# Optimization experiments

Hardware: AMD Instinct MI355X
Metric: run time of the kernel (lower is better)

## Reference

```python
import jax, jax.numpy as jnp
import numpy as np

B, T_HIST, D_IN = 4096, 60, 2
H, L, T_OUT = 128, 2, 360


def _lstm_cell(x, h, c, Wih, Whh, b):
    # PyTorch gate order: i, f, g, o
    z = x @ Wih.T + h @ Whh.T + b  # (B, 4H)
    i, f, g, o = jnp.split(z, 4, axis=-1)
    c_new = jax.nn.sigmoid(f) * c + jax.nn.sigmoid(i) * jnp.tanh(g)
    h_new = jax.nn.sigmoid(o) * jnp.tanh(c_new)
    return h_new, c_new


def _multilayer_step(x_t, hs, cs, Wih, Whh, b):
    # hs, cs: (L, B, H); Wih: (L, 4H, H); Whh: (L, 4H, H); b: (L, 4H)
    new_h, new_c = [], []
    inp = x_t
    for l in range(L):
        h, c = _lstm_cell(inp, hs[l], cs[l], Wih[l], Whh[l], b[l])
        new_h.append(h)
        new_c.append(c)
        inp = h
    return inp, jnp.stack(new_h), jnp.stack(new_c)


def setup_inputs() -> dict:
    key = jax.random.key(0)
    ks = jax.random.split(key, 14)
    s = 0.1
    inp = {
        "history": jax.random.normal(ks[0], (B, T_HIST, D_IN), jnp.float32),
        "emb_W": jax.random.normal(ks[1], (H, D_IN), jnp.float32) * s,
        "emb_b": jax.random.normal(ks[2], (H,), jnp.float32) * s,
        "enc_Wih": jax.random.normal(ks[3], (L, 4 * H, H), jnp.float32) * s,
        "enc_Whh": jax.random.normal(ks[4], (L, 4 * H, H), jnp.float32) * s,
        "enc_bih": jax.random.normal(ks[5], (L, 4 * H), jnp.float32) * s,
        "enc_bhh": jax.random.normal(ks[6], (L, 4 * H), jnp.float32) * s,
        "dec_Wih": jax.random.normal(ks[7], (L, 4 * H, H), jnp.float32) * s,
        "dec_Whh": jax.random.normal(ks[8], (L, 4 * H, H), jnp.float32) * s,
        "dec_bih": jax.random.normal(ks[9], (L, 4 * H), jnp.float32) * s,
        "dec_bhh": jax.random.normal(ks[10], (L, 4 * H), jnp.float32) * s,
        "out_W": jax.random.normal(ks[11], (D_IN, H), jnp.float32) * s,
        "out_b": jax.random.normal(ks[12], (D_IN,), jnp.float32) * s,
    }
    return inp


def reference(history, emb_W, emb_b, enc_Wih, enc_Whh, enc_bih, enc_bhh,
              dec_Wih, dec_Whh, dec_bih, dec_bhh, out_W, out_b):
    batch = history.shape[0]
    enc_b = enc_bih + enc_bhh  # (L, 4H)
    dec_b = dec_bih + dec_bhh

    # input embedding: (B, T, 2) -> (B, T, H)
    hist_embed = history @ emb_W.T + emb_b

    # --- encoder LSTM (eval mode, no dropout) ---
    h0 = jnp.zeros((L, batch, H), hist_embed.dtype)
    c0 = jnp.zeros((L, batch, H), hist_embed.dtype)

    def enc_step(carry, x_t):
        hs, cs = carry
        _, hs, cs = _multilayer_step(x_t, hs, cs, enc_Wih, enc_Whh, enc_b)
        return (hs, cs), None

    (h_n, c_n), _ = jax.lax.scan(enc_step, (h0, c0),
                                 jnp.transpose(hist_embed, (1, 0, 2)))  # scan over time

    dec_in0 = jnp.zeros((batch, H), hist_embed.dtype)

    def dec_step(carry, _):
        dec_in, hs, cs = carry
        top, hs, cs = _multilayer_step(dec_in, hs, cs, dec_Wih, dec_Whh, dec_b)
        pred = top @ out_W.T + out_b              # (B, 2)
        nxt = pred @ emb_W.T + emb_b              # re-embed prediction
        return (nxt, hs, cs), pred

    _, preds = jax.lax.scan(dec_step, (dec_in0, h_n, c_n), None, length=T_OUT)
    return jnp.transpose(preds, (1, 0, 2))  # (B, T_OUT, 2)
```

## Files before the change

### kernel.cpp

```cpp
#include <hip/hip_runtime.h>
#include <stdint.h>

#define NT 512

typedef __attribute__((ext_vector_type(8))) __bf16 bf16x8;
typedef __attribute__((ext_vector_type(8))) unsigned short ushort8;
typedef __attribute__((ext_vector_type(4))) float f32x4;

static __device__ __forceinline__ unsigned short f2bf(float f) {
    union { float f; uint32_t u; } v; v.f = f;
    uint32_t r = v.u + 0x7fffu + ((v.u >> 16) & 1u);
    return (unsigned short)(r >> 16);
}
static __device__ __forceinline__ float sigm(float x) {
    return __builtin_amdgcn_rcpf(1.0f + __expf(-x));
}
static __device__ __forceinline__ float tanh_(float x) {
    return 2.0f * __builtin_amdgcn_rcpf(1.0f + __expf(-2.0f * x)) - 1.0f;
}
static __device__ __forceinline__ bf16x8 ld8(const unsigned short* p) {
    return __builtin_bit_cast(bf16x8, *(const ushort8*)p);
}
static __device__ __forceinline__ float swz(float v, int imm) {
    int r;
    if (imm == 0x0010) r = __builtin_amdgcn_ds_swizzle(__builtin_bit_cast(int, v), 0x0010);
    else               r = __builtin_amdgcn_ds_swizzle(__builtin_bit_cast(int, v), 0x0410);
    return __builtin_bit_cast(float, r);
}

__global__ void prep_kernel(
    const float* __restrict__ emb_W, const float* __restrict__ emb_b,
    const float* __restrict__ enc_Wih, const float* __restrict__ enc_Whh,
    const float* __restrict__ dec_Wih, const float* __restrict__ dec_Whh,
    const float* __restrict__ enc_bih, const float* __restrict__ enc_bhh,
    const float* __restrict__ dec_bih, const float* __restrict__ dec_bhh,
    unsigned short* __restrict__ W0p, unsigned short* __restrict__ W1p,
    float* __restrict__ benc, float* __restrict__ bdec,
    float* __restrict__ Me, float* __restrict__ Md,
    float* __restrict__ ve, float* __restrict__ vd)
{
    int idx = blockIdx.x * blockDim.x + threadIdx.x;
    if (idx < 2 * 512 * 256) {
        int net = idx >> 17;
        int rem = idx & 131071;
        int n = rem >> 8, k = rem & 255;
        const float* Wih = net ? dec_Wih : enc_Wih;
        const float* Whh = net ? dec_Whh : enc_Whh;
        float v = (k < 128) ? Wih[(size_t)(512 + n) * 128 + k]
                            : Whh[(size_t)(512 + n) * 128 + k - 128];
        W1p[(size_t)net * 131072 + rem] = f2bf(v);
    }
    if (idx < 2 * 512 * 128) {
        int net = idx >> 16;
        int rem = idx & 65535;
        int j = rem & 7, quad = (rem >> 3) & 3, ln = (rem >> 5) & 15;
        int w = (rem >> 9) & 7, g = (rem >> 12) & 3, c = (rem >> 14) & 3;
        int n = g * 128 + w * 16 + ln;
        int k = c * 32 + quad * 8 + j;
        const float* Whh = net ? dec_Whh : enc_Whh;
        W0p[(size_t)net * 65536 + rem] = f2bf(Whh[(size_t)n * 128 + k]);
    }
    if (idx < 2048) {
        int net = idx >> 10;
        int rem = idx & 1023;
        float v = net ? (dec_bih[rem] + dec_bhh[rem]) : (enc_bih[rem] + enc_bhh[rem]);
        (net ? bdec : benc)[rem] = v;
    }
    if (idx < 1024) {
        int net = idx >> 9, n = idx & 511;
        const float* Wih = net ? dec_Wih : enc_Wih;
        float m0 = 0.f, m1 = 0.f, vv = 0.f;
        for (int k = 0; k < 128; ++k) {
            float wv = Wih[(size_t)n * 128 + k];
            m0 += wv * emb_W[k * 2 + 0];
            m1 += wv * emb_W[k * 2 + 1];
            vv += wv * emb_b[k];
        }
        float* M = net ? Md : Me;
        float* V = net ? vd : ve;
        M[n * 2 + 0] = m0; M[n * 2 + 1] = m1; V[n] = vv;
    }
}

__global__ __launch_bounds__(NT, 2) void lstm_kernel(
    const float* __restrict__ hist,
    const unsigned short* __restrict__ W0p, const unsigned short* __restrict__ W1p,
    const float* __restrict__ benc, const float* __restrict__ bdec,
    const float* __restrict__ Me, const float* __restrict__ Md,
    const float* __restrict__ ve, const float* __restrict__ vd,
    const float* __restrict__ out_W, const float* __restrict__ out_b,
    float* __restrict__ out)
{
    __shared__ __align__(16) unsigned short A1s[2 * 4096];
    __shared__ __align__(16) unsigned short W0Ls[65536];
    __shared__ __align__(16) float histL[16 * 120];

    const int tid = threadIdx.x;
    const int lane = tid & 63;
    const int w = tid >> 6;
    const int ln = lane & 15;
    const int quad = lane >> 4;
    const int row0 = blockIdx.x * 16;
    const int cc0 = w * 16 + ln;
    const int cg = (cc0 >> 3) & 3;

    const unsigned short* a1r = A1s + ln * 32 + ((quad ^ ((ln >> 2) & 3)) * 8);
    unsigned short* a1w = A1s + (cc0 >> 5) * 512 + quad * 128 + ((cg ^ quad) * 8) + (ln & 7);
    const unsigned short* w0b[4];
#pragma unroll
    for (int c = 0; c < 4; ++c)
        w0b[c] = W0Ls + c * 16384 + w * 512 + ln * 32 + quad * 8;

    for (int e = tid; e < 1024; e += NT) ((uint4*)A1s)[e] = make_uint4(0u, 0u, 0u, 0u);
    for (int e = tid; e < 480; e += NT)
        ((float4*)histL)[e] = ((const float4*)(hist + (size_t)row0 * 120))[e];

    const int nidx = (ln < 2) ? ln : 0;
    const float outbL = out_b[nidx];
    bf16x8 ow[4];
#pragma unroll
    for (int c = 0; c < 4; ++c) {
        unsigned short tmp[8];
#pragma unroll
        for (int j = 0; j < 8; ++j)
            tmp[j] = f2bf(out_W[nidx * 128 + c * 32 + quad * 8 + j]);
        ow[c] = __builtin_bit_cast(bf16x8, *(ushort8*)tmp);
    }

    bf16x8 wl[4][8];
    float b0c[4], bvc[4], b1c[4], M0c[4], M1c[4];
    float c0r[4] = {0.f, 0.f, 0.f, 0.f};
    float c1r[4] = {0.f, 0.f, 0.f, 0.f};

    auto load_consts = [&](const float* bb, const float* M, const float* V,
                           const unsigned short* W1) {
#pragma unroll
        for (int g = 0; g < 4; ++g) {
            const int n = g * 128 + cc0;
#pragma unroll
            for (int q = 0; q < 8; ++q)
                wl[g][q] = ld8(W1 + (size_t)n * 256 + quad * 8 + q * 32);
            b0c[g] = bb[n];
            b1c[g] = bb[512 + n];
            M0c[g] = M[n * 2 + 0];
            M1c[g] = M[n * 2 + 1];
            bvc[g] = bb[n] + V[n];
        }
    };
    auto copy_w0 = [&](const unsigned short* src) {
        for (int e = tid; e < 8192; e += NT)
            ((uint4*)W0Ls)[e] = ((const uint4*)src)[e];
    };

    copy_w0(W0p);
    load_consts(benc, Me, ve, W1p);
    __syncthreads();

    auto enc_step = [&](int t, int buf) {
        bf16x8 a0[4];
#pragma unroll
        for (int c = 0; c < 4; ++c)
            a0[c] = ld8(a1r + (buf ^ 1) * 4096 + c * 512);
        f32x4 acc[4];
#pragma unroll
        for (int g = 0; g < 4; ++g)
#pragma unroll
            for (int i = 0; i < 4; ++i) {
                float2 pv = *(const float2*)&histL[(quad * 4 + i) * 120 + 2 * t];
                acc[g][i] = bvc[g] + M0c[g] * pv.x + M1c[g] * pv.y;
            }
#pragma unroll
        for (int c = 0; c < 4; ++c)
#pragma unroll
            for (int g = 0; g < 4; ++g)
                acc[g] = __builtin_amdgcn_mfma_f32_16x16x32_bf16(a0[c], ld8(w0b[c] + g * 4096), acc[g], 0, 0, 0);
#pragma unroll
        for (int i = 0; i < 4; ++i) {
            float iv = sigm(acc[0][i]);
            float fv = sigm(acc[1][i]);
            float gv = tanh_(acc[2][i]);
            float ov = sigm(acc[3][i]);
            c0r[i] = fv * c0r[i] + iv * gv;
            a1w[buf * 4096 + i * 32] = f2bf(ov * tanh_(c0r[i]));
        }
        __syncthreads();
        f32x4 acc1[4];
#pragma unroll
        for (int g = 0; g < 4; ++g)
#pragma unroll
            for (int i = 0; i < 4; ++i) acc1[g][i] = b1c[g];
#pragma unroll
        for (int q = 0; q < 8; ++q) {
            bf16x8 af = ld8(a1r + buf * 4096 + q * 512);
#pragma unroll
            for (int g = 0; g < 4; ++g)
                acc1[g] = __builtin_amdgcn_mfma_f32_16x16x32_bf16(af, wl[g][q], acc1[g], 0, 0, 0);
        }
#pragma unroll
        for (int i = 0; i < 4; ++i) {
            float iv = sigm(acc1[0][i]);
            float fv = sigm(acc1[1][i]);
            float gv = tanh_(acc1[2][i]);
            float ov = sigm(acc1[3][i]);
            c1r[i] = fv * c1r[i] + iv * gv;
            a1w[(buf ^ 1) * 4096 + 2048 + i * 32] = f2bf(ov * tanh_(c1r[i]));
        }
        __syncthreads();
    };

    for (int t = 0; t < 60; t += 2) { enc_step(t, 0); enc_step(t + 1, 1); }

    copy_w0(W0p + 65536);
    load_consts(bdec, Md, vd, W1p + 131072);
    __syncthreads();

    auto dec_step = [&](int d, int buf) {
        f32x4 acc[4];
        if (d > 0) {
            f32x4 pacc = {0.f, 0.f, 0.f, 0.f};
#pragma unroll
            for (int c = 0; c < 4; ++c) {
                bf16x8 ah = ld8(a1r + buf * 4096 + (4 + c) * 512);
                pacc = __builtin_amdgcn_mfma_f32_16x16x32_bf16(ah, ow[c], pacc, 0, 0, 0);
            }
            float pd[4];
#pragma unroll
            for (int i = 0; i < 4; ++i) pd[i] = pacc[i] + outbL;
            if (w == 0 && ln < 2) {
#pragma unroll
                for (int i = 0; i < 4; ++i)
                    out[(size_t)(row0 + quad * 4 + i) * 720 + (size_t)(d - 1) * 2 + ln] = pd[i];
            }
#pragma unroll
            for (int g = 0; g < 4; ++g)
#pragma unroll
                for (int i = 0; i < 4; ++i) acc[g][i] = bvc[g];
#pragma unroll
            for (int i = 0; i < 4; ++i) {
                float p0 = swz(pd[i], 0x0010);
                float p1 = swz(pd[i], 0x0410);
#pragma unroll
                for (int g = 0; g < 4; ++g)
                    acc[g][i] += M0c[g] * p0 + M1c[g] * p1;
            }
        } else {
#pragma unroll
            for (int g = 0; g < 4; ++g)
#pragma unroll
                for (int i = 0; i < 4; ++i) acc[g][i] = b0c[g];
        }
        bf16x8 a0[4];
#pragma unroll
        for (int c = 0; c < 4; ++c)
            a0[c] = ld8(a1r + (buf ^ 1) * 4096 + c * 512);
#pragma unroll
        for (int c = 0; c < 4; ++c)
#pragma unroll
            for (int g = 0; g < 4; ++g)
                acc[g] = __builtin_amdgcn_mfma_f32_16x16x32_bf16(a0[c], ld8(w0b[c] + g * 4096), acc[g], 0, 0, 0);
#pragma unroll
        for (int i = 0; i < 4; ++i) {
            float iv = sigm(acc[0][i]);
            float fv = sigm(acc[1][i]);
            float gv = tanh_(acc[2][i]);
            float ov = sigm(acc[3][i]);
            c0r[i] = fv * c0r[i] + iv * gv;
            a1w[buf * 4096 + i * 32] = f2bf(ov * tanh_(c0r[i]));
        }
        __syncthreads();
        f32x4 acc1[4];
#pragma unroll
        for (int g = 0; g < 4; ++g)
#pragma unroll
            for (int i = 0; i < 4; ++i) acc1[g][i] = b1c[g];
#pragma unroll
        for (int q = 0; q < 8; ++q) {
            bf16x8 af = ld8(a1r + buf * 4096 + q * 512);
#pragma unroll
            for (int g = 0; g < 4; ++g)
                acc1[g] = __builtin_amdgcn_mfma_f32_16x16x32_bf16(af, wl[g][q], acc1[g], 0, 0, 0);
        }
#pragma unroll
        for (int i = 0; i < 4; ++i) {
            float iv = sigm(acc1[0][i]);
            float fv = sigm(acc1[1][i]);
            float gv = tanh_(acc1[2][i]);
            float ov = sigm(acc1[3][i]);
            c1r[i] = fv * c1r[i] + iv * gv;
            a1w[(buf ^ 1) * 4096 + 2048 + i * 32] = f2bf(ov * tanh_(c1r[i]));
        }
        __syncthreads();
    };

    for (int d = 0; d < 360; d += 2) { dec_step(d, 0); dec_step(d + 1, 1); }

    {
        f32x4 pacc = {0.f, 0.f, 0.f, 0.f};
#pragma unroll
        for (int c = 0; c < 4; ++c) {
            bf16x8 ah = ld8(a1r + 0 * 4096 + (4 + c) * 512);
            pacc = __builtin_amdgcn_mfma_f32_16x16x32_bf16(ah, ow[c], pacc, 0, 0, 0);
        }
        if (w == 0 && ln < 2) {
#pragma unroll
            for (int i = 0; i < 4; ++i)
                out[(size_t)(row0 + quad * 4 + i) * 720 + 359 * 2 + ln] = pacc[i] + outbL;
        }
    }
}

extern "C" void kernel_launch(void* const* d_in, const int* in_sizes, int n_in,
                              void* d_out, int out_size, void* d_ws, size_t ws_size,
                              hipStream_t stream) {
    const float* hist    = (const float*)d_in[0];
    const float* emb_W   = (const float*)d_in[1];
    const float* emb_b   = (const float*)d_in[2];
    const float* enc_Wih = (const float*)d_in[3];
    const float* enc_Whh = (const float*)d_in[4];
    const float* enc_bih = (const float*)d_in[5];
    const float* enc_bhh = (const float*)d_in[6];
    const float* dec_Wih = (const float*)d_in[7];
    const float* dec_Whh = (const float*)d_in[8];
    const float* dec_bih = (const float*)d_in[9];
    const float* dec_bhh = (const float*)d_in[10];
    const float* out_W   = (const float*)d_in[11];
    const float* out_b   = (const float*)d_in[12];

    char* ws = (char*)d_ws;
    unsigned short* W0p = (unsigned short*)(ws + 0);
    unsigned short* W1p = (unsigned short*)(ws + 262144);
    float* benc = (float*)(ws + 786432);
    float* bdec = (float*)(ws + 790528);
    float* Me   = (float*)(ws + 794624);
    float* Md   = (float*)(ws + 798720);
    float* ve   = (float*)(ws + 802816);
    float* vd   = (float*)(ws + 804864);

    prep_kernel<<<1024, 256, 0, stream>>>(emb_W, emb_b,
                                          enc_Wih, enc_Whh, dec_Wih, dec_Whh,
                                          enc_bih, enc_bhh, dec_bih, dec_bhh,
                                          W0p, W1p, benc, bdec, Me, Md, ve, vd);
    lstm_kernel<<<256, NT, 0, stream>>>(hist, W0p, W1p,
                                        benc, bdec, Me, Md, ve, vd,
                                        out_W, out_b, (float*)d_out);
}
```

Measured before the change: 1.214 ms.

## Skew LSTM layers across timesteps and swizzle layer-0 weight LDS layout

Restructures the recurrence so each step computes layer 1 at time t and layer 0 at time t+1 from the same loaded hidden-state fragments. In the encoder this removes one barrier per step. The decoder keeps two barriers per step, but the layer-0 weight MFMA now overlaps the layer-1 work and only the small projection and embedding fixup stays on the serial path. It also XOR-swizzles the layer-0 weight layout in LDS to reduce bank conflicts, and adds prologue and epilogue code for the skewed schedule, which raises complexity and the chance of indexing errors.

```diff
diff --git a/kernel.cpp b/kernel.cpp
--- a/kernel.cpp
+++ b/kernel.cpp
@@ -109,9 +109,9 @@
     const unsigned short* w0b[4];
 #pragma unroll
     for (int c = 0; c < 4; ++c)
-        w0b[c] = W0Ls + c * 16384 + w * 512 + ln * 32 + quad * 8;
-
-    for (int e = tid; e < 1024; e += NT) ((uint4*)A1s)[e] = make_uint4(0u, 0u, 0u, 0u);
+        w0b[c] = W0Ls + c * 16384 + w * 512 + ln * 32 + ((quad ^ ((ln >> 1) & 3)) * 8);
+
+    for (int e = tid; e < 256; e += NT) ((uint4*)A1s)[256 + e] = make_uint4(0u, 0u, 0u, 0u);
     for (int e = tid; e < 480; e += NT)
         ((float4*)histL)[e] = ((const float4*)(hist + (size_t)row0 * 120))[e];
 
@@ -148,54 +148,64 @@
         }
     };
     auto copy_w0 = [&](const unsigned short* src) {
-        for (int e = tid; e < 8192; e += NT)
-            ((uint4*)W0Ls)[e] = ((const uint4*)src)[e];
+        for (int e = tid; e < 8192; e += NT) {
+            int d = (e & ~3) | ((e & 3) ^ ((e >> 3) & 3));
+            ((uint4*)W0Ls)[d] = ((const uint4*)src)[e];
+        }
     };
 
     copy_w0(W0p);
     load_consts(benc, Me, ve, W1p);
     __syncthreads();
 
+    {
+        f32x4 z[4];
+#pragma unroll
+        for (int i = 0; i < 4; ++i) {
+            float x0 = hist[(size_t)(row0 + quad * 4 + i) * 120 + 0];
+            float x1 = hist[(size_t)(row0 + quad * 4 + i) * 120 + 1];
+#pragma unroll
+            for (int g = 0; g < 4; ++g) z[g][i] = bvc[g] + M0c[g] * x0 + M1c[g] * x1;
+        }
+#pragma unroll
+        for (int i = 0; i < 4; ++i) {
+            float iv = sigm(z[0][i]);
+            float gv = tanh_(z[2][i]);
+            float ov = sigm(z[3][i]);
+            c0r[i] = iv * gv;
+            a1w[i * 32] = f2bf(ov * tanh_(c0r[i]));
+        }
+    }
+    __syncthreads();
+
     auto enc_step = [&](int t, int buf) {
-        bf16x8 a0[4];
+        bf16x8 af[8];
+#pragma unroll
+        for (int q = 0; q < 8; ++q)
+            af[q] = ld8(a1r + buf * 4096 + q * 512);
+        f32x4 acc1[4];
+#pragma unroll
+        for (int g = 0; g < 4; ++g)
+#pragma unroll
+            for (int i = 0; i < 4; ++i) acc1[g][i] = b1c[g];
+#pragma unroll
+        for (int q = 0; q < 8; ++q)
+#pragma unroll
+            for (int g = 0; g < 4; ++g)
+                acc1[g] = __builtin_amdgcn_mfma_f32_16x16x32_bf16(af[q], wl[g][q], acc1[g], 0, 0, 0);
+        f32x4 acc0[4];
+#pragma unroll
+        for (int g = 0; g < 4; ++g)
+#pragma unroll
+            for (int i = 0; i < 4; ++i) {
+                float2 pv = *(const float2*)&histL[(quad * 4 + i) * 120 + 2 * (t + 1)];
+                acc0[g][i] = bvc[g] + M0c[g] * pv.x + M1c[g] * pv.y;
+            }
 #pragma unroll
         for (int c = 0; c < 4; ++c)
-            a0[c] = ld8(a1r + (buf ^ 1) * 4096 + c * 512);
-        f32x4 acc[4];
-#pragma unroll
-        for (int g = 0; g < 4; ++g)
-#pragma unroll
-            for (int i = 0; i < 4; ++i) {
-                float2 pv = *(const float2*)&histL[(quad * 4 + i) * 120 + 2 * t];
-                acc[g][i] = bvc[g] + M0c[g] * pv.x + M1c[g] * pv.y;
-            }
-#pragma unroll
-        for (int c = 0; c < 4; ++c)
-#pragma unroll
-            for (int g = 0; g < 4; ++g)
-                acc[g] = __builtin_amdgcn_mfma_f32_16x16x32_bf16(a0[c], ld8(w0b[c] + g * 4096), acc[g], 0, 0, 0);
-#pragma unroll
-        for (int i = 0; i < 4; ++i) {
-            float iv = sigm(acc[0][i]);
-            float fv = sigm(acc[1][i]);
-            float gv = tanh_(acc[2][i]);
-            float ov = sigm(acc[3][i]);
-            c0r[i] = fv * c0r[i] + iv * gv;
-            a1w[buf * 4096 + i * 32] = f2bf(ov * tanh_(c0r[i]));
-        }
-        __syncthreads();
-        f32x4 acc1[4];
-#pragma unroll
-        for (int g = 0; g < 4; ++g)
-#pragma unroll
-            for (int i = 0; i < 4; ++i) acc1[g][i] = b1c[g];
-#pragma unroll
-        for (int q = 0; q < 8; ++q) {
-            bf16x8 af = ld8(a1r + buf * 4096 + q * 512);
-#pragma unroll
-            for (int g = 0; g < 4; ++g)
-                acc1[g] = __builtin_amdgcn_mfma_f32_16x16x32_bf16(af, wl[g][q], acc1[g], 0, 0, 0);
-        }
+#pragma unroll
+            for (int g = 0; g < 4; ++g)
+                acc0[g] = __builtin_amdgcn_mfma_f32_16x16x32_bf16(af[c], ld8(w0b[c] + g * 4096), acc0[g], 0, 0, 0);
 #pragma unroll
         for (int i = 0; i < 4; ++i) {
             float iv = sigm(acc1[0][i]);
@@ -205,81 +215,91 @@
             c1r[i] = fv * c1r[i] + iv * gv;
             a1w[(buf ^ 1) * 4096 + 2048 + i * 32] = f2bf(ov * tanh_(c1r[i]));
         }
+#pragma unroll
+        for (int i = 0; i < 4; ++i) {
+            float iv = sigm(acc0[0][i]);
+            float fv = sigm(acc0[1][i]);
+            float gv = tanh_(acc0[2][i]);
+            float ov = sigm(acc0[3][i]);
+            c0r[i] = fv * c0r[i] + iv * gv;
+            a1w[(buf ^ 1) * 4096 + i * 32] = f2bf(ov * tanh_(c0r[i]));
+        }
         __syncthreads();
     };
 
-    for (int t = 0; t < 60; t += 2) { enc_step(t, 0); enc_step(t + 1, 1); }
-
-    copy_w0(W0p + 65536);
-    load_consts(bdec, Md, vd, W1p + 131072);
-    __syncthreads();
+    for (int t = 0; t < 58; t += 2) { enc_step(t, 0); enc_step(t + 1, 1); }
+    enc_step(58, 0);
+
+    {
+        bf16x8 af[8];
+#pragma unroll
+        for (int q = 0; q < 8; ++q)
+            af[q] = ld8(a1r + 4096 + q * 512);
+        f32x4 acc1[4];
+#pragma unroll
+        for (int g = 0; g < 4; ++g)
+#pragma unroll
+            for (int i = 0; i < 4; ++i) acc1[g][i] = b1c[g];
+#pragma unroll
+        for (int q = 0; q < 8; ++q)
+#pragma unroll
+            for (int g = 0; g < 4; ++g)
+                acc1[g] = __builtin_amdgcn_mfma_f32_16x16x32_bf16(af[q], wl[g][q], acc1[g], 0, 0, 0);
+#pragma unroll
+        for (int i = 0; i < 4; ++i) {
+            float iv = sigm(acc1[0][i]);
+            float fv = sigm(acc1[1][i]);
+            float gv = tanh_(acc1[2][i]);
+            float ov = sigm(acc1[3][i]);
+            c1r[i] = fv * c1r[i] + iv * gv;
+            a1w[2048 + i * 32] = f2bf(ov * tanh_(c1r[i]));
+        }
+        copy_w0(W0p + 65536);
+        load_consts(bdec, Md, vd, W1p + 131072);
+        __syncthreads();
+        f32x4 acc0[4];
+#pragma unroll
+        for (int g = 0; g < 4; ++g) acc0[g] = (f32x4){0.f, 0.f, 0.f, 0.f};
+#pragma unroll
+        for (int c = 0; c < 4; ++c)
+#pragma unroll
+            for (int g = 0; g < 4; ++g)
+                acc0[g] = __builtin_amdgcn_mfma_f32_16x16x32_bf16(af[c], ld8(w0b[c] + g * 4096), acc0[g], 0, 0, 0);
+#pragma unroll
+        for (int i = 0; i < 4; ++i) {
+            float iv = sigm(acc0[0][i] + b0c[0]);
+            float fv = sigm(acc0[1][i] + b0c[1]);
+            float gv = tanh_(acc0[2][i] + b0c[2]);
+            float ov = sigm(acc0[3][i] + b0c[3]);
+            c0r[i] = fv * c0r[i] + iv * gv;
+            a1w[i * 32] = f2bf(ov * tanh_(c0r[i]));
+        }
+        __syncthreads();
+    }
 
     auto dec_step = [&](int d, int buf) {
-        f32x4 acc[4];
-        if (d > 0) {
-            f32x4 pacc = {0.f, 0.f, 0.f, 0.f};
-#pragma unroll
-            for (int c = 0; c < 4; ++c) {
-                bf16x8 ah = ld8(a1r + buf * 4096 + (4 + c) * 512);
-                pacc = __builtin_amdgcn_mfma_f32_16x16x32_bf16(ah, ow[c], pacc, 0, 0, 0);
-            }
-            float pd[4];
-#pragma unroll
-            for (int i = 0; i < 4; ++i) pd[i] = pacc[i] + outbL;
-            if (w == 0 && ln < 2) {
-#pragma unroll
-                for (int i = 0; i < 4; ++i)
-                    out[(size_t)(row0 + quad * 4 + i) * 720 + (size_t)(d - 1) * 2 + ln] = pd[i];
-            }
-#pragma unroll
-            for (int g = 0; g < 4; ++g)
-#pragma unroll
-                for (int i = 0; i < 4; ++i) acc[g][i] = bvc[g];
-#pragma unroll
-            for (int i = 0; i < 4; ++i) {
-                float p0 = swz(pd[i], 0x0010);
-                float p1 = swz(pd[i], 0x0410);
-#pragma unroll
-                for (int g = 0; g < 4; ++g)
-                    acc[g][i] += M0c[g] * p0 + M1c[g] * p1;
-            }
-        } else {
-#pragma unroll
-            for (int g = 0; g < 4; ++g)
-#pragma unroll
-                for (int i = 0; i < 4; ++i) acc[g][i] = b0c[g];
-        }
-        bf16x8 a0[4];
+        bf16x8 af[8];
+#pragma unroll
+        for (int q = 0; q < 8; ++q)
+            af[q] = ld8(a1r + buf * 4096 + q * 512);
+        f32x4 acc1[4];
+#pragma unroll
+        for (int g = 0; g < 4; ++g)
+#pragma unroll
+            for (int i = 0; i < 4; ++i) acc1[g][i] = b1c[g];
+#pragma unroll
+        for (int q = 0; q < 8; ++q)
+#pragma unroll
+            for (int g = 0; g < 4; ++g)
+                acc1[g] = __builtin_amdgcn_mfma_f32_16x16x32_bf16(af[q], wl[g][q], acc1[g], 0, 0, 0);
+        f32x4 acc0[4];
+#pragma unroll
+        for (int g = 0; g < 4; ++g) acc0[g] = (f32x4){0.f, 0.f, 0.f, 0.f};
 #pragma unroll
         for (int c = 0; c < 4; ++c)
-            a0[c] = ld8(a1r + (buf ^ 1) * 4096 + c * 512);
-#pragma unroll
-        for (int c = 0; c < 4; ++c)
-#pragma unroll
-            for (int g = 0; g < 4; ++g)
-                acc[g] = __builtin_amdgcn_mfma_f32_16x16x32_bf16(a0[c], ld8(w0b[c] + g * 4096), acc[g], 0, 0, 0);
-#pragma unroll
-        for (int i = 0; i < 4; ++i) {
-            float iv = sigm(acc[0][i]);
-            float fv = sigm(acc[1][i]);
-            float gv = tanh_(acc[2][i]);
-            float ov = sigm(acc[3][i]);
-            c0r[i] = fv * c0r[i] + iv * gv;
-            a1w[buf * 4096 + i * 32] = f2bf(ov * tanh_(c0r[i]));
-        }
-        __syncthreads();
-        f32x4 acc1[4];
-#pragma unroll
-        for (int g = 0; g < 4; ++g)
-#pragma unroll
-            for (int i = 0; i < 4; ++i) acc1[g][i] = b1c[g];
-#pragma unroll
-        for (int q = 0; q < 8; ++q) {
-            bf16x8 af = ld8(a1r + buf * 4096 + q * 512);
-#pragma unroll
-            for (int g = 0; g < 4; ++g)
-                acc1[g] = __builtin_amdgcn_mfma_f32_16x16x32_bf16(af, wl[g][q], acc1[g], 0, 0, 0);
-        }
+#pragma unroll
+            for (int g = 0; g < 4; ++g)
+                acc0[g] = __builtin_amdgcn_mfma_f32_16x16x32_bf16(af[c], ld8(w0b[c] + g * 4096), acc0[g], 0, 0, 0);
 #pragma unroll
         for (int i = 0; i < 4; ++i) {
             float iv = sigm(acc1[0][i]);
@@ -290,23 +310,38 @@
             a1w[(buf ^ 1) * 4096 + 2048 + i * 32] = f2bf(ov * tanh_(c1r[i]));
         }
         __syncthreads();
+        f32x4 pa = {0.f, 0.f, 0.f, 0.f}, pb = {0.f, 0.f, 0.f, 0.f};
+        pa = __builtin_amdgcn_mfma_f32_16x16x32_bf16(ld8(a1r + (buf ^ 1) * 4096 + 4 * 512), ow[0], pa, 0, 0, 0);
+        pb = __builtin_amdgcn_mfma_f32_16x16x32_bf16(ld8(a1r + (buf ^ 1) * 4096 + 5 * 512), ow[1], pb, 0, 0, 0);
+        pa = __builtin_amdgcn_mfma_f32_16x16x32_bf16(ld8(a1r + (buf ^ 1) * 4096 + 6 * 512), ow[2], pa, 0, 0, 0);
+        pb = __builtin_amdgcn_mfma_f32_16x16x32_bf16(ld8(a1r + (buf ^ 1) * 4096 + 7 * 512), ow[3], pb, 0, 0, 0);
+        float pd[4];
+#pragma unroll
+        for (int i = 0; i < 4; ++i) pd[i] = pa[i] + pb[i] + outbL;
+        if (w == 0 && ln < 2) {
+#pragma unroll
+            for (int i = 0; i < 4; ++i)
+                out[(size_t)(row0 + quad * 4 + i) * 720 + (size_t)d * 2 + ln] = pd[i];
+        }
+#pragma unroll
+        for (int i = 0; i < 4; ++i) {
+            float p0 = swz(pd[i], 0x0010);
+            float p1 = swz(pd[i], 0x0410);
+            float z0 = acc0[0][i] + bvc[0] + M0c[0] * p0 + M1c[0] * p1;
+            float z1 = acc0[1][i] + bvc[1] + M0c[1] * p0 + M1c[1] * p1;
+            float z2 = acc0[2][i] + bvc[2] + M0c[2] * p0 + M1c[2] * p1;
+            float z3 = acc0[3][i] + bvc[3] + M0c[3] * p0 + M1c[3] * p1;
+            float iv = sigm(z0);
+            float fv = sigm(z1);
+            float gv = tanh_(z2);
+            float ov = sigm(z3);
+            c0r[i] = fv * c0r[i] + iv * gv;
+            a1w[(buf ^ 1) * 4096 + i * 32] = f2bf(ov * tanh_(c0r[i]));
+        }
+        __syncthreads();
     };
 
     for (int d = 0; d < 360; d += 2) { dec_step(d, 0); dec_step(d + 1, 1); }
-
-    {
-        f32x4 pacc = {0.f, 0.f, 0.f, 0.f};
-#pragma unroll
-        for (int c = 0; c < 4; ++c) {
-            bf16x8 ah = ld8(a1r + 0 * 4096 + (4 + c) * 512);
-            pacc = __builtin_amdgcn_mfma_f32_16x16x32_bf16(ah, ow[c], pacc, 0, 0, 0);
-        }
-        if (w == 0 && ln < 2) {
-#pragma unroll
-            for (int i = 0; i < 4; ++i)
-                out[(size_t)(row0 + quad * 4 + i) * 720 + 359 * 2 + ln] = pacc[i] + outbL;
-        }
-    }
 }
 
 extern "C" void kernel_launch(void* const* d_in, const int* in_sizes, int n_in,
```

After: 1.025 ms. 15.6% less time.
